# Kernel tuning notes

Hardware: AMD Instinct MI355X
Metric: run time of the kernel (lower is better)

## Reference

```python
import jax, jax.numpy as jnp
import numpy as np

N_NODES = 50000
N_EDGES = 400000
D_IN = 64
D_HID = 64
D_OUT = 64
NEG_SLOPE = 0.2   # GATConv LeakyReLU slope
BN_EPS = 1e-5


def _add_self_loops(row, col, N):
    loop = jnp.arange(N, dtype=row.dtype)
    return jnp.concatenate([row, loop]), jnp.concatenate([col, loop])


def _gcn_conv(x, row, col, N, W, b):
    # PyG GCNConv: add self loops, symmetric normalization, sum aggregate, bias
    r, c = _add_self_loops(row, col, N)
    deg = jax.ops.segment_sum(jnp.ones_like(r, dtype=x.dtype), c, num_segments=N)
    dis = jnp.where(deg > 0, deg ** -0.5, 0.0)
    norm = dis[r] * dis[c]                       # [E+N]
    h = x @ W                                    # [N, out]
    out = jax.ops.segment_sum(h[r] * norm[:, None], c, num_segments=N)
    return out + b


def _gat_conv(x, row, col, N, W, att_src, att_dst, b, concat):
    # PyG GATConv: per-edge attention with softmax over incoming edges
    H, C = att_src.shape
    r, c = _add_self_loops(row, col, N)
    h = (x @ W).reshape(N, H, C)
    a_src = jnp.einsum('nhc,hc->nh', h, att_src)
    a_dst = jnp.einsum('nhc,hc->nh', h, att_dst)
    e = jax.nn.leaky_relu(a_src[r] + a_dst[c], NEG_SLOPE)   # [E', H]
    m = jax.ops.segment_max(e, c, num_segments=N)           # stable softmax per target
    e = jnp.exp(e - m[c])
    denom = jax.ops.segment_sum(e, c, num_segments=N)
    alpha = e / denom[c]                                    # [E', H]
    out = jax.ops.segment_sum(h[r] * alpha[:, :, None], c, num_segments=N)  # [N,H,C]
    out = out.reshape(N, H * C) if concat else out.mean(axis=1)
    return out + b


def _sage_conv(x, row, col, N, Wl, bl, Wr):
    # PyG SAGEConv(aggr='mean', normalize=True): lin_l(mean_j x_j) + lin_r(x), then L2-normalize
    s = jax.ops.segment_sum(x[row], col, num_segments=N)
    cnt = jax.ops.segment_sum(jnp.ones_like(row, dtype=x.dtype), col, num_segments=N)
    mean = s / jnp.maximum(cnt, 1.0)[:, None]
    out = mean @ Wl + bl + x @ Wr
    n = jnp.linalg.norm(out, axis=-1, keepdims=True)
    return out / jnp.maximum(n, 1e-12)


def _forward(x, edge_index, gate_w1, gate_b1, gate_w2, gate_b2,
             gcn_w1, gcn_b1, bn_gamma, bn_beta, gcn_w2, gcn_b2,
             gat_w1, gat_att_src1, gat_att_dst1, gat_b1,
             gat_w2, gat_att_src2, gat_att_dst2, gat_b2,
             sage_wl1, sage_bl1, sage_wr1, sage_wl2, sage_bl2, sage_wr2):
    N = x.shape[0]
    row, col = edge_index[0], edge_index[1]
    # gate: mean node feature -> MLP -> softmax over 3 models
    g = jnp.mean(x, axis=0, keepdims=True)
    w = jax.nn.softmax(jax.nn.relu(g @ gate_w1 + gate_b1) @ gate_w2 + gate_b2, axis=-1)
    # GCN branch (eval: BatchNorm with running mean=0, var=1; dropout off)
    h = _gcn_conv(x, row, col, N, gcn_w1, gcn_b1)
    h = h * (bn_gamma / jnp.sqrt(1.0 + BN_EPS)) + bn_beta
    h = jax.nn.relu(h)
    out_gcn = _gcn_conv(h, row, col, N, gcn_w2, gcn_b2)
    # GAT branch: hidden layer 4 heads concat + ELU, output layer 1 head mean
    h = jax.nn.elu(_gat_conv(x, row, col, N, gat_w1, gat_att_src1, gat_att_dst1, gat_b1, True))
    out_gat = _gat_conv(h, row, col, N, gat_w2, gat_att_src2, gat_att_dst2, gat_b2, False)
    # SAGE branch
    h = jax.nn.relu(_sage_conv(x, row, col, N, sage_wl1, sage_bl1, sage_wr1))
    out_sage = _sage_conv(h, row, col, N, sage_wl2, sage_bl2, sage_wr2)
    return w[0, 0] * out_gcn + w[0, 1] * out_gat + w[0, 2] * out_sage


def setup_inputs() -> dict:
    key = jax.random.key(0)
    ks = jax.random.split(key, 16)
    def nrm(k, shape, scale=0.05):
        return jax.random.normal(k, shape, dtype=jnp.float32) * scale
    inp = {}
    inp['x'] = jax.random.normal(ks[0], (N_NODES, D_IN), dtype=jnp.float32)
    inp['edge_index'] = jax.random.randint(ks[1], (2, N_EDGES), 0, N_NODES, dtype=jnp.int32)
    inp['gate_w1'] = nrm(ks[2], (D_IN, 64)); inp['gate_b1'] = jnp.zeros((64,), jnp.float32)
    inp['gate_w2'] = nrm(ks[3], (64, 3));    inp['gate_b2'] = jnp.zeros((3,), jnp.float32)
    inp['gcn_w1'] = nrm(ks[4], (D_IN, D_HID)); inp['gcn_b1'] = jnp.zeros((D_HID,), jnp.float32)
    inp['bn_gamma'] = jnp.ones((D_HID,), jnp.float32); inp['bn_beta'] = jnp.zeros((D_HID,), jnp.float32)
    inp['gcn_w2'] = nrm(ks[5], (D_HID, D_OUT)); inp['gcn_b2'] = jnp.zeros((D_OUT,), jnp.float32)
    inp['gat_w1'] = nrm(ks[6], (D_IN, 4 * D_HID))
    inp['gat_att_src1'] = nrm(ks[7], (4, D_HID)); inp['gat_att_dst1'] = nrm(ks[8], (4, D_HID))
    inp['gat_b1'] = jnp.zeros((4 * D_HID,), jnp.float32)
    inp['gat_w2'] = nrm(ks[9], (4 * D_HID, D_OUT))
    inp['gat_att_src2'] = nrm(ks[10], (1, D_OUT)); inp['gat_att_dst2'] = nrm(ks[11], (1, D_OUT))
    inp['gat_b2'] = jnp.zeros((D_OUT,), jnp.float32)
    inp['sage_wl1'] = nrm(ks[12], (D_IN, D_HID)); inp['sage_bl1'] = jnp.zeros((D_HID,), jnp.float32)
    inp['sage_wr1'] = nrm(ks[13], (D_IN, D_HID))
    inp['sage_wl2'] = nrm(ks[14], (D_HID, D_OUT)); inp['sage_bl2'] = jnp.zeros((D_OUT,), jnp.float32)
    inp['sage_wr2'] = nrm(ks[15], (D_HID, D_OUT))
    return inp


def reference(x, edge_index, gate_w1, gate_b1, gate_w2, gate_b2,
              gcn_w1, gcn_b1, bn_gamma, bn_beta, gcn_w2, gcn_b2,
              gat_w1, gat_att_src1, gat_att_dst1, gat_b1,
              gat_w2, gat_att_src2, gat_att_dst2, gat_b2,
              sage_wl1, sage_bl1, sage_wr1, sage_wl2, sage_bl2, sage_wr2):
    return _forward(x, edge_index, gate_w1, gate_b1, gate_w2, gate_b2,
                    gcn_w1, gcn_b1, bn_gamma, bn_beta, gcn_w2, gcn_b2,
                    gat_w1, gat_att_src1, gat_att_dst1, gat_b1,
                    gat_w2, gat_att_src2, gat_att_dst2, gat_b2,
                    sage_wl1, sage_bl1, sage_wr1, sage_wl2, sage_bl2, sage_wr2)
```

## Files before the change

### kernel.cpp

```cpp
#include <hip/hip_runtime.h>
#include <hip/hip_bf16.h>
#include <math.h>

#define NN 50000
#define NE 400000

typedef __attribute__((ext_vector_type(8))) short bf16x8;
typedef __attribute__((ext_vector_type(4))) float f32x4;

__device__ __forceinline__ float lrelu(float v){ return v > 0.f ? v : 0.2f*v; }
__device__ __forceinline__ float elu1(float v){ return v > 0.f ? v : expm1f(v); }
__device__ __forceinline__ float bflo(unsigned int u){ return __uint_as_float(u << 16); }
__device__ __forceinline__ float bfhi(unsigned int u){ return __uint_as_float(u & 0xffff0000u); }
__device__ __forceinline__ unsigned short f2bf(float f){
  __hip_bfloat16 h = __float2bfloat16(f);
  return *(unsigned short*)&h;
}
__device__ __forceinline__ unsigned int pack2(float lo, float hi){
  return (unsigned int)f2bf(lo) | ((unsigned int)f2bf(hi) << 16);
}

__device__ __forceinline__ void stage_tab(unsigned short* Wt, const unsigned short* Wb, int tid){
  #pragma unroll
  for(int s = 0; s < 2; s++){
    int c = tid + s*256;
    int n = c >> 3, ko = (c & 7)*8;
    *(bf16x8*)&Wt[n*72 + ko] = *(const bf16x8*)&Wb[n*64 + ko];
  }
}

__global__ void k_count(const int* __restrict__ col, int* __restrict__ cnt, int E){
  int e = blockIdx.x*blockDim.x + threadIdx.x;
  if(e < E) atomicAdd(&cnt[col[e]], 1);
}

__global__ void k_alloc(const int* __restrict__ cnt, int* __restrict__ offs,
                        float* __restrict__ dis, float* __restrict__ invc,
                        int* __restrict__ total, int N){
  int i = blockIdx.x*blockDim.x + threadIdx.x;
  int lane = threadIdx.x & 63;
  int v = (i < N) ? cnt[i] : 0;
  int x = v;
  #pragma unroll
  for(int d = 1; d < 64; d <<= 1){ int t = __shfl_up(x, d, 64); if(lane >= d) x += t; }
  int base = 0;
  if(lane == 63 && x > 0) base = atomicAdd(total, x);
  base = __shfl(base, 63, 64);
  if(i < N){
    offs[i] = base + x - v;
    dis[i]  = 1.0f / sqrtf((float)(v + 1));
    invc[i] = 1.0f / fmaxf((float)v, 1.0f);
  }
}

__global__ void k_fill(const int* __restrict__ row, const int* __restrict__ col,
                       const int* __restrict__ offs, int* __restrict__ cursor,
                       int* __restrict__ csr, int E){
  int e = blockIdx.x*blockDim.x + threadIdx.x;
  if(e < E){
    int c = col[e];
    int pos = offs[c] + atomicAdd(&cursor[c], 1);
    csr[pos] = row[e];
  }
}

struct PKS { const float* src; unsigned short* dst; int kshift; int ldw; int col0; };
struct PKP { PKS s[11]; };

__global__ void k_packw(PKP p){
  PKS s = p.s[blockIdx.x];
  int K = 1 << s.kshift;
  int total = K << 6;
  for(int idx = threadIdx.x; idx < total; idx += 256){
    int n = idx >> s.kshift, k = idx & (K - 1);
    s.dst[idx] = f2bf(s.src[(size_t)k*s.ldw + s.col0 + n]);
  }
}

__global__ void k_castsum(const float* __restrict__ x, unsigned short* __restrict__ xb,
                          float* __restrict__ gsum, int N){
  __shared__ float part[4][64];
  int lane = threadIdx.x & 63, w = threadIdx.x >> 6;
  float s = 0.f;
  for(int r = blockIdx.x*4 + w; r < N; r += gridDim.x*4){
    float v = x[(size_t)r*64 + lane];
    xb[(size_t)r*64 + lane] = f2bf(v);
    s += v;
  }
  part[w][lane] = s;
  __syncthreads();
  if(w == 0) atomicAdd(&gsum[lane], part[0][lane]+part[1][lane]+part[2][lane]+part[3][lane]);
}

__global__ void k_gate(const float* __restrict__ gsum,
                       const float* __restrict__ w1, const float* __restrict__ b1,
                       const float* __restrict__ w2, const float* __restrict__ b2,
                       float* __restrict__ gatew){
  __shared__ float g[64]; __shared__ float hid[64]; __shared__ float lg[3];
  int t = threadIdx.x;
  g[t] = gsum[t] * (1.0f/(float)NN);
  __syncthreads();
  float acc = b1[t];
  for(int i = 0; i < 64; i++) acc += g[i]*w1[i*64 + t];
  hid[t] = fmaxf(acc, 0.f);
  __syncthreads();
  if(t < 3){
    float a = b2[t];
    for(int j = 0; j < 64; j++) a += hid[j]*w2[j*3 + t];
    lg[t] = a;
  }
  __syncthreads();
  if(t == 0){
    float m = fmaxf(lg[0], fmaxf(lg[1], lg[2]));
    float e0 = expf(lg[0]-m), e1 = expf(lg[1]-m), e2 = expf(lg[2]-m);
    float s = e0 + e1 + e2;
    gatew[0] = e0/s; gatew[1] = e1/s; gatew[2] = e2/s;
  }
}

__global__ void k_fold1(const float* __restrict__ w1, const float* __restrict__ as,
                        const float* __restrict__ ad, float* __restrict__ wsd){
  int t = threadIdx.x;
  int k = t & 63, h = t >> 6;
  float ssrc = 0.f, sdst = 0.f;
  for(int c = 0; c < 64; c++){
    float w = w1[k*256 + h*64 + c];
    ssrc += w * as[h*64 + c];
    sdst += w * ad[h*64 + c];
  }
  wsd[k*8 + h] = ssrc;
  wsd[k*8 + 4 + h] = sdst;
}

__global__ void k_attdotx(const unsigned short* __restrict__ xb, const float* __restrict__ wsd,
                          float* __restrict__ asrc, float* __restrict__ adst, int N){
  __shared__ float ws[64*8];
  int tid = threadIdx.x;
  ws[tid] = wsd[tid];
  ws[tid + 256] = wsd[tid + 256];
  __syncthreads();
  int node = blockIdx.x*16 + (tid >> 4);
  int l = tid & 15;
  if(node >= N) return;
  uint2 u = *(const uint2*)&xb[(size_t)node*64 + l*4];
  float v0 = bflo(u.x), v1 = bfhi(u.x), v2 = bflo(u.y), v3 = bfhi(u.y);
  float s[8];
  #pragma unroll
  for(int h = 0; h < 8; h++){
    s[h] = v0*ws[(l*4+0)*8+h] + v1*ws[(l*4+1)*8+h] + v2*ws[(l*4+2)*8+h] + v3*ws[(l*4+3)*8+h];
  }
  #pragma unroll
  for(int d = 8; d >= 1; d >>= 1){
    #pragma unroll
    for(int h = 0; h < 8; h++) s[h] += __shfl_xor(s[h], d, 16);
  }
  if(l == 0){
    float4 o1; o1.x = s[0]; o1.y = s[1]; o1.z = s[2]; o1.w = s[3];
    float4 o2; o2.x = s[4]; o2.y = s[5]; o2.z = s[6]; o2.w = s[7];
    *(float4*)&asrc[node*4] = o1;
    *(float4*)&adst[node*4] = o2;
  }
}

__global__ void k_edgew1(const float* __restrict__ asrc, const float* __restrict__ adst,
                         const int* __restrict__ offs, const int* __restrict__ cnt,
                         const int* __restrict__ csr,
                         float* __restrict__ wvE, float* __restrict__ rdenN,
                         float* __restrict__ wvS, int N){
  int node = blockIdx.x*4 + (threadIdx.x >> 6);
  int lane = threadIdx.x & 63;
  if(node >= N) return;
  float4 ad = *(const float4*)&adst[node*4];
  float a0 = 0.f, a1 = 0.f, a2 = 0.f, a3 = 0.f;
  int e0 = offs[node], e1 = e0 + cnt[node];
  for(int e = e0 + lane; e < e1; e += 64){
    int s = csr[e];
    float4 as = *(const float4*)&asrc[s*4];
    float4 w;
    w.x = expf(lrelu(as.x + ad.x));
    w.y = expf(lrelu(as.y + ad.y));
    w.z = expf(lrelu(as.z + ad.z));
    w.w = expf(lrelu(as.w + ad.w));
    a0 += w.x; a1 += w.y; a2 += w.z; a3 += w.w;
    *(float4*)&wvE[(size_t)e*4] = w;
  }
  #pragma unroll
  for(int d = 32; d >= 1; d >>= 1){
    a0 += __shfl_xor(a0, d, 64); a1 += __shfl_xor(a1, d, 64);
    a2 += __shfl_xor(a2, d, 64); a3 += __shfl_xor(a3, d, 64);
  }
  float4 asl = *(const float4*)&asrc[node*4];
  float4 ws;
  ws.x = expf(lrelu(asl.x + ad.x));
  ws.y = expf(lrelu(asl.y + ad.y));
  ws.z = expf(lrelu(asl.z + ad.z));
  ws.w = expf(lrelu(asl.w + ad.w));
  if(lane == 0){
    float4 rd;
    rd.x = 1.0f/(a0 + ws.x); rd.y = 1.0f/(a1 + ws.y);
    rd.z = 1.0f/(a2 + ws.z); rd.w = 1.0f/(a3 + ws.w);
    *(float4*)&rdenN[node*4] = rd;
    *(float4*)&wvS[node*4] = ws;
  }
}

__global__ void k_edgew2(const float* __restrict__ asrc, const float* __restrict__ adst,
                         const int* __restrict__ offs, const int* __restrict__ cnt,
                         const int* __restrict__ csr,
                         float* __restrict__ wvE, float* __restrict__ rdenN,
                         float* __restrict__ wvS, int N){
  int node = blockIdx.x*4 + (threadIdx.x >> 6);
  int lane = threadIdx.x & 63;
  if(node >= N) return;
  float ad = adst[node];
  float acc = 0.f;
  int e0 = offs[node], e1 = e0 + cnt[node];
  for(int e = e0 + lane; e < e1; e += 64){
    float w = expf(lrelu(asrc[csr[e]] + ad));
    acc += w;
    wvE[e] = w;
  }
  #pragma unroll
  for(int d = 32; d >= 1; d >>= 1) acc += __shfl_xor(acc, d, 64);
  float ws = expf(lrelu(asrc[node] + ad));
  if(lane == 0){
    rdenN[node] = 1.0f/(acc + ws);
    wvS[node] = ws;
  }
}

__global__ void k_aggx(const unsigned short* __restrict__ xb,
                       const float* __restrict__ wvE, const float* __restrict__ rden,
                       const float* __restrict__ wvS,
                       const float* __restrict__ dis, const float* __restrict__ invc,
                       const int* __restrict__ offs, const int* __restrict__ cnt,
                       const int* __restrict__ csr,
                       unsigned short* __restrict__ z, unsigned short* __restrict__ agcnx,
                       unsigned short* __restrict__ asagex, int N){
  int node = blockIdx.x*4 + (threadIdx.x >> 6);
  int lane = threadIdx.x & 63;
  if(node >= N) return;
  int half = lane >> 5, subl = lane & 31;
  float zg[4][2] = {{0,0},{0,0},{0,0},{0,0}};
  float gg[2] = {0,0}, ssv[2] = {0,0};
  int e0 = offs[node], e1 = e0 + cnt[node];
  #pragma unroll 2
  for(int e = e0 + half; e < e1; e += 2){
    int s = csr[e];
    float4 w4 = *(const float4*)&wvE[(size_t)e*4];
    float ds = dis[s];
    unsigned int u = *(const unsigned int*)&xb[(size_t)s*64 + subl*2];
    float xl = bflo(u), xh = bfhi(u);
    zg[0][0] = fmaf(w4.x, xl, zg[0][0]); zg[0][1] = fmaf(w4.x, xh, zg[0][1]);
    zg[1][0] = fmaf(w4.y, xl, zg[1][0]); zg[1][1] = fmaf(w4.y, xh, zg[1][1]);
    zg[2][0] = fmaf(w4.z, xl, zg[2][0]); zg[2][1] = fmaf(w4.z, xh, zg[2][1]);
    zg[3][0] = fmaf(w4.w, xl, zg[3][0]); zg[3][1] = fmaf(w4.w, xh, zg[3][1]);
    gg[0] = fmaf(ds, xl, gg[0]); gg[1] = fmaf(ds, xh, gg[1]);
    ssv[0] += xl; ssv[1] += xh;
  }
  #pragma unroll
  for(int h = 0; h < 4; h++){
    zg[h][0] += __shfl_xor(zg[h][0], 32, 64);
    zg[h][1] += __shfl_xor(zg[h][1], 32, 64);
  }
  gg[0] += __shfl_xor(gg[0], 32, 64); gg[1] += __shfl_xor(gg[1], 32, 64);
  ssv[0] += __shfl_xor(ssv[0], 32, 64); ssv[1] += __shfl_xor(ssv[1], 32, 64);
  if(half == 0){
    unsigned int un = *(const unsigned int*)&xb[(size_t)node*64 + subl*2];
    float xl = bflo(un), xh = bfhi(un);
    float4 ws4 = *(const float4*)&wvS[node*4];
    float4 rd4 = *(const float4*)&rden[node*4];
    unsigned int* zp = (unsigned int*)&z[(size_t)node*256 + subl*2];
    zp[0]   = pack2((zg[0][0] + ws4.x*xl)*rd4.x, (zg[0][1] + ws4.x*xh)*rd4.x);
    zp[32]  = pack2((zg[1][0] + ws4.y*xl)*rd4.y, (zg[1][1] + ws4.y*xh)*rd4.y);
    zp[64]  = pack2((zg[2][0] + ws4.z*xl)*rd4.z, (zg[2][1] + ws4.z*xh)*rd4.z);
    zp[96]  = pack2((zg[3][0] + ws4.w*xl)*rd4.w, (zg[3][1] + ws4.w*xh)*rd4.w);
    float dc = dis[node], ic = invc[node];
    *(unsigned int*)&agcnx[(size_t)node*64 + subl*2] =
        pack2(dc*fmaf(dc, xl, gg[0]), dc*fmaf(dc, xh, gg[1]));
    *(unsigned int*)&asagex[(size_t)node*64 + subl*2] = pack2(ssv[0]*ic, ssv[1]*ic);
  }
}

__global__ void k_aggf(const unsigned short* __restrict__ a1, const unsigned short* __restrict__ s1,
                       const unsigned short* __restrict__ h2,
                       const float* __restrict__ wvE, const float* __restrict__ rden,
                       const float* __restrict__ wvS,
                       const float* __restrict__ dis, const float* __restrict__ invc,
                       const int* __restrict__ offs, const int* __restrict__ cnt,
                       const int* __restrict__ csr,
                       unsigned short* __restrict__ A2agg, unsigned short* __restrict__ S2agg,
                       unsigned short* __restrict__ T2, int N){
  int node = blockIdx.x*4 + (threadIdx.x >> 6);
  int lane = threadIdx.x & 63;
  if(node >= N) return;
  int half = lane >> 5, subl = lane & 31;
  float aa[2] = {0,0}, ss[2] = {0,0}, tt[2] = {0,0};
  int e0 = offs[node], e1 = e0 + cnt[node];
  #pragma unroll 2
  for(int e = e0 + half; e < e1; e += 2){
    int s = csr[e];
    float ds = dis[s];
    float wv = wvE[e];
    unsigned int ua = *(const unsigned int*)&a1[(size_t)s*64 + subl*2];
    unsigned int us = *(const unsigned int*)&s1[(size_t)s*64 + subl*2];
    unsigned int uh = *(const unsigned int*)&h2[(size_t)s*64 + subl*2];
    aa[0] = fmaf(ds, bflo(ua), aa[0]); aa[1] = fmaf(ds, bfhi(ua), aa[1]);
    ss[0] += bflo(us); ss[1] += bfhi(us);
    tt[0] = fmaf(wv, bflo(uh), tt[0]); tt[1] = fmaf(wv, bfhi(uh), tt[1]);
  }
  aa[0] += __shfl_xor(aa[0], 32, 64); aa[1] += __shfl_xor(aa[1], 32, 64);
  ss[0] += __shfl_xor(ss[0], 32, 64); ss[1] += __shfl_xor(ss[1], 32, 64);
  tt[0] += __shfl_xor(tt[0], 32, 64); tt[1] += __shfl_xor(tt[1], 32, 64);
  if(half == 0){
    unsigned int uan = *(const unsigned int*)&a1[(size_t)node*64 + subl*2];
    unsigned int uhn = *(const unsigned int*)&h2[(size_t)node*64 + subl*2];
    float dc = dis[node], ic = invc[node];
    float rd = rden[node], wss = wvS[node];
    *(unsigned int*)&A2agg[(size_t)node*64 + subl*2] =
        pack2(dc*fmaf(dc, bflo(uan), aa[0]), dc*fmaf(dc, bfhi(uan), aa[1]));
    *(unsigned int*)&S2agg[(size_t)node*64 + subl*2] = pack2(ss[0]*ic, ss[1]*ic);
    *(unsigned int*)&T2[(size_t)node*64 + subl*2] =
        pack2(fmaf(wss, bflo(uhn), tt[0])*rd, fmaf(wss, bfhi(uhn), tt[1])*rd);
  }
}

struct MME {
  const unsigned short* A; const unsigned short* Wb;
  const unsigned short* A2; const unsigned short* Wb2;
  unsigned short* C;
  const float* b; const float* p1; const float* p2;
  int ep;
};
struct FSP {
  const unsigned short* z; const unsigned short* wb1; const float* b1;
  const unsigned short* wb2; const float* as2; const float* ad2;
  unsigned short* h2; float* asrc2; float* adst2;
  MME mm[2];
  int N;
};

__global__ __launch_bounds__(256, 4) void k_fused1(FSP p){
  __shared__ unsigned short smem[16896];
  const int N = p.N;
  int tid = threadIdx.x;
  int w = tid >> 6, lane = tid & 63, quad = lane >> 4, m16 = lane & 15;
  int rowa = blockIdx.x*64 + w*16 + m16;
  int rowc = rowa < N ? rowa : N - 1;
  int robase = blockIdx.x*64 + w*16 + quad*4;

  if(blockIdx.y == 0){
    unsigned short* GH = smem;
    int lr = w*16;
    #pragma unroll
    for(int h = 0; h < 4; h++){
      bf16x8 a0 = *(const bf16x8*)&p.z[(size_t)rowc*256 + h*64 + quad*8];
      bf16x8 a1 = *(const bf16x8*)&p.z[(size_t)rowc*256 + h*64 + 32 + quad*8];
      f32x4 acc[4];
      #pragma unroll
      for(int t = 0; t < 4; t++){ acc[t][0]=0.f; acc[t][1]=0.f; acc[t][2]=0.f; acc[t][3]=0.f; }
      #pragma unroll
      for(int t = 0; t < 4; t++){
        const unsigned short* wb = p.wb1 + (size_t)h*4096 + (t*16 + m16)*64;
        bf16x8 b0 = *(const bf16x8*)&wb[quad*8];
        bf16x8 b1v = *(const bf16x8*)&wb[32 + quad*8];
        acc[t] = __builtin_amdgcn_mfma_f32_16x16x32_bf16(a0, b0, acc[t], 0, 0, 0);
        acc[t] = __builtin_amdgcn_mfma_f32_16x16x32_bf16(a1, b1v, acc[t], 0, 0, 0);
      }
      #pragma unroll
      for(int t = 0; t < 4; t++){
        float bv = p.b1[h*64 + t*16 + m16];
        #pragma unroll
        for(int r = 0; r < 4; r++){
          GH[(lr + quad*4 + r)*264 + h*64 + t*16 + m16] = f2bf(elu1(acc[t][r] + bv));
        }
      }
    }
    __syncthreads();
    f32x4 acc2[4];
    #pragma unroll
    for(int t = 0; t < 4; t++){ acc2[t][0]=0.f; acc2[t][1]=0.f; acc2[t][2]=0.f; acc2[t][3]=0.f; }
    #pragma unroll
    for(int kc = 0; kc < 256; kc += 64){
      bf16x8 a0 = *(const bf16x8*)&GH[(lr + m16)*264 + kc + quad*8];
      bf16x8 a1 = *(const bf16x8*)&GH[(lr + m16)*264 + kc + 32 + quad*8];
      #pragma unroll
      for(int t = 0; t < 4; t++){
        const unsigned short* wb = p.wb2 + (size_t)(t*16 + m16)*256 + kc;
        bf16x8 b0 = *(const bf16x8*)&wb[quad*8];
        bf16x8 b1v = *(const bf16x8*)&wb[32 + quad*8];
        acc2[t] = __builtin_amdgcn_mfma_f32_16x16x32_bf16(a0, b0, acc2[t], 0, 0, 0);
        acc2[t] = __builtin_amdgcn_mfma_f32_16x16x32_bf16(a1, b1v, acc2[t], 0, 0, 0);
      }
    }
    #pragma unroll
    for(int t = 0; t < 4; t++){
      int col = t*16 + m16;
      #pragma unroll
      for(int r = 0; r < 4; r++){
        int ro = robase + r;
        if(ro < N) p.h2[(size_t)ro*64 + col] = f2bf(acc2[t][r]);
      }
    }
    float ps[4] = {0,0,0,0}, pd[4] = {0,0,0,0};
    #pragma unroll
    for(int t = 0; t < 4; t++){
      int col = t*16 + m16;
      float a_ = p.as2[col], d_ = p.ad2[col];
      #pragma unroll
      for(int r = 0; r < 4; r++){ ps[r] = fmaf(acc2[t][r], a_, ps[r]); pd[r] = fmaf(acc2[t][r], d_, pd[r]); }
    }
    #pragma unroll
    for(int d = 8; d >= 1; d >>= 1){
      #pragma unroll
      for(int r = 0; r < 4; r++){ ps[r] += __shfl_xor(ps[r], d, 64); pd[r] += __shfl_xor(pd[r], d, 64); }
    }
    if(m16 == 0){
      #pragma unroll
      for(int r = 0; r < 4; r++){
        int ro = robase + r;
        if(ro < N){ p.asrc2[ro] = ps[r]; p.adst2[ro] = pd[r]; }
      }
    }
    return;
  }

  MME m = p.mm[blockIdx.y - 1];
  unsigned short* Wt  = smem;
  unsigned short* Wt2 = smem + 4608;
  stage_tab(Wt, m.Wb, tid);
  if(m.Wb2) stage_tab(Wt2, m.Wb2, tid);
  __syncthreads();
  f32x4 acc[4];
  #pragma unroll
  for(int t = 0; t < 4; t++){ acc[t][0]=0.f; acc[t][1]=0.f; acc[t][2]=0.f; acc[t][3]=0.f; }
  {
    bf16x8 a0 = *(const bf16x8*)&m.A[(size_t)rowc*64 + quad*8];
    bf16x8 a1 = *(const bf16x8*)&m.A[(size_t)rowc*64 + 32 + quad*8];
    #pragma unroll
    for(int t = 0; t < 4; t++){
      bf16x8 b0 = *(const bf16x8*)&Wt[(t*16 + m16)*72 + quad*8];
      bf16x8 b1 = *(const bf16x8*)&Wt[(t*16 + m16)*72 + 32 + quad*8];
      acc[t] = __builtin_amdgcn_mfma_f32_16x16x32_bf16(a0, b0, acc[t], 0, 0, 0);
      acc[t] = __builtin_amdgcn_mfma_f32_16x16x32_bf16(a1, b1, acc[t], 0, 0, 0);
    }
  }
  if(m.A2){
    bf16x8 a0 = *(const bf16x8*)&m.A2[(size_t)rowc*64 + quad*8];
    bf16x8 a1 = *(const bf16x8*)&m.A2[(size_t)rowc*64 + 32 + quad*8];
    #pragma unroll
    for(int t = 0; t < 4; t++){
      bf16x8 b0 = *(const bf16x8*)&Wt2[(t*16 + m16)*72 + quad*8];
      bf16x8 b1 = *(const bf16x8*)&Wt2[(t*16 + m16)*72 + 32 + quad*8];
      acc[t] = __builtin_amdgcn_mfma_f32_16x16x32_bf16(a0, b0, acc[t], 0, 0, 0);
      acc[t] = __builtin_amdgcn_mfma_f32_16x16x32_bf16(a1, b1, acc[t], 0, 0, 0);
    }
  }
  if(m.ep == 3){
    float v[4][4], n2[4] = {0,0,0,0};
    #pragma unroll
    for(int t = 0; t < 4; t++){
      float bv = m.b[t*16 + m16];
      #pragma unroll
      for(int r = 0; r < 4; r++){ v[t][r] = acc[t][r] + bv; n2[r] = fmaf(v[t][r], v[t][r], n2[r]); }
    }
    #pragma unroll
    for(int d = 8; d >= 1; d >>= 1){
      #pragma unroll
      for(int r = 0; r < 4; r++) n2[r] += __shfl_xor(n2[r], d, 64);
    }
    float inv[4];
    #pragma unroll
    for(int r = 0; r < 4; r++) inv[r] = 1.0f / fmaxf(sqrtf(n2[r]), 1e-12f);
    #pragma unroll
    for(int t = 0; t < 4; t++){
      #pragma unroll
      for(int r = 0; r < 4; r++){
        int ro = robase + r;
        if(ro < N) m.C[(size_t)ro*64 + t*16 + m16] = f2bf(fmaxf(v[t][r]*inv[r], 0.f));
      }
    }
    return;
  }
  #pragma unroll
  for(int t = 0; t < 4; t++){
    int col = t*16 + m16;
    float bv = m.b[col];
    float gm = m.p1[col]*rsqrtf(1.0f + 1e-5f);
    float be = m.p2[col];
    #pragma unroll
    for(int r = 0; r < 4; r++){
      int ro = robase + r;
      if(ro < N){
        m.C[(size_t)ro*64 + col] = f2bf(fmaxf((acc[t][r] + bv)*gm + be, 0.f));
      }
    }
  }
}

__global__ __launch_bounds__(256) void k_mm_final(
    const unsigned short* __restrict__ A2agg, const unsigned short* __restrict__ wb_gcn2,
    const float* __restrict__ gcn_b2,
    const unsigned short* __restrict__ S2agg, const unsigned short* __restrict__ wb_wl2,
    const float* __restrict__ bl2,
    const unsigned short* __restrict__ s1, const unsigned short* __restrict__ wb_wr2,
    const unsigned short* __restrict__ T2, const float* __restrict__ gat_b2,
    const float* __restrict__ gatew, float* __restrict__ out, int N){
  __shared__ unsigned short W1s[64*72];
  __shared__ unsigned short W2s[64*72];
  __shared__ unsigned short W3s[64*72];
  int tid = threadIdx.x;
  stage_tab(W1s, wb_gcn2, tid);
  stage_tab(W2s, wb_wl2, tid);
  stage_tab(W3s, wb_wr2, tid);
  __syncthreads();
  int w = tid >> 6, lane = tid & 63, quad = lane >> 4, m16 = lane & 15;
  int rowa = blockIdx.x*64 + w*16 + m16;
  int rowc = rowa < N ? rowa : N - 1;
  f32x4 accg[4], accs[4];
  #pragma unroll
  for(int t = 0; t < 4; t++){
    accg[t][0]=0.f; accg[t][1]=0.f; accg[t][2]=0.f; accg[t][3]=0.f;
    accs[t][0]=0.f; accs[t][1]=0.f; accs[t][2]=0.f; accs[t][3]=0.f;
  }
  {
    bf16x8 a0 = *(const bf16x8*)&A2agg[(size_t)rowc*64 + quad*8];
    bf16x8 a1 = *(const bf16x8*)&A2agg[(size_t)rowc*64 + 32 + quad*8];
    #pragma unroll
    for(int t = 0; t < 4; t++){
      bf16x8 b0 = *(const bf16x8*)&W1s[(t*16 + m16)*72 + quad*8];
      bf16x8 b1 = *(const bf16x8*)&W1s[(t*16 + m16)*72 + 32 + quad*8];
      accg[t] = __builtin_amdgcn_mfma_f32_16x16x32_bf16(a0, b0, accg[t], 0, 0, 0);
      accg[t] = __builtin_amdgcn_mfma_f32_16x16x32_bf16(a1, b1, accg[t], 0, 0, 0);
    }
  }
  {
    bf16x8 a0 = *(const bf16x8*)&S2agg[(size_t)rowc*64 + quad*8];
    bf16x8 a1 = *(const bf16x8*)&S2agg[(size_t)rowc*64 + 32 + quad*8];
    #pragma unroll
    for(int t = 0; t < 4; t++){
      bf16x8 b0 = *(const bf16x8*)&W2s[(t*16 + m16)*72 + quad*8];
      bf16x8 b1 = *(const bf16x8*)&W2s[(t*16 + m16)*72 + 32 + quad*8];
      accs[t] = __builtin_amdgcn_mfma_f32_16x16x32_bf16(a0, b0, accs[t], 0, 0, 0);
      accs[t] = __builtin_amdgcn_mfma_f32_16x16x32_bf16(a1, b1, accs[t], 0, 0, 0);
    }
  }
  {
    bf16x8 a0 = *(const bf16x8*)&s1[(size_t)rowc*64 + quad*8];
    bf16x8 a1 = *(const bf16x8*)&s1[(size_t)rowc*64 + 32 + quad*8];
    #pragma unroll
    for(int t = 0; t < 4; t++){
      bf16x8 b0 = *(const bf16x8*)&W3s[(t*16 + m16)*72 + quad*8];
      bf16x8 b1 = *(const bf16x8*)&W3s[(t*16 + m16)*72 + 32 + quad*8];
      accs[t] = __builtin_amdgcn_mfma_f32_16x16x32_bf16(a0, b0, accs[t], 0, 0, 0);
      accs[t] = __builtin_amdgcn_mfma_f32_16x16x32_bf16(a1, b1, accs[t], 0, 0, 0);
    }
  }
  float w0 = gatew[0], w1 = gatew[1], w2 = gatew[2];
  int robase = blockIdx.x*64 + w*16 + quad*4;
  float vs[4][4], n2[4] = {0,0,0,0};
  #pragma unroll
  for(int t = 0; t < 4; t++){
    float bsv = bl2[t*16 + m16];
    #pragma unroll
    for(int r = 0; r < 4; r++){ vs[t][r] = accs[t][r] + bsv; n2[r] = fmaf(vs[t][r], vs[t][r], n2[r]); }
  }
  #pragma unroll
  for(int d = 8; d >= 1; d >>= 1){
    #pragma unroll
    for(int r = 0; r < 4; r++) n2[r] += __shfl_xor(n2[r], d, 64);
  }
  float inv[4];
  #pragma unroll
  for(int r = 0; r < 4; r++) inv[r] = 1.0f / fmaxf(sqrtf(n2[r]), 1e-12f);
  #pragma unroll
  for(int t = 0; t < 4; t++){
    int col = t*16 + m16;
    float bg = gcn_b2[col], bt = gat_b2[col];
    #pragma unroll
    for(int r = 0; r < 4; r++){
      int ro = robase + r;
      if(ro < N){
        float t2 = bflo((unsigned int)T2[(size_t)ro*64 + col]);
        out[(size_t)ro*64 + col] = w0*(accg[t][r] + bg) + w1*(t2 + bt) + w2*vs[t][r]*inv[r];
      }
    }
  }
}

extern "C" void kernel_launch(void* const* d_in, const int* in_sizes, int n_in,
                              void* d_out, int out_size, void* d_ws, size_t ws_size,
                              hipStream_t stream){
  const float* x        = (const float*)d_in[0];
  const int*   ei       = (const int*)d_in[1];
  const int*   row      = ei;
  const int*   col      = ei + NE;
  const float* gate_w1  = (const float*)d_in[2];
  const float* gate_b1  = (const float*)d_in[3];
  const float* gate_w2  = (const float*)d_in[4];
  const float* gate_b2  = (const float*)d_in[5];
  const float* gcn_w1   = (const float*)d_in[6];
  const float* gcn_b1   = (const float*)d_in[7];
  const float* bn_gamma = (const float*)d_in[8];
  const float* bn_beta  = (const float*)d_in[9];
  const float* gcn_w2   = (const float*)d_in[10];
  const float* gcn_b2   = (const float*)d_in[11];
  const float* gat_w1   = (const float*)d_in[12];
  const float* gat_as1  = (const float*)d_in[13];
  const float* gat_ad1  = (const float*)d_in[14];
  const float* gat_b1   = (const float*)d_in[15];
  const float* gat_w2   = (const float*)d_in[16];
  const float* gat_as2  = (const float*)d_in[17];
  const float* gat_ad2  = (const float*)d_in[18];
  const float* gat_b2   = (const float*)d_in[19];
  const float* sage_wl1 = (const float*)d_in[20];
  const float* sage_bl1 = (const float*)d_in[21];
  const float* sage_wr1 = (const float*)d_in[22];
  const float* sage_wl2 = (const float*)d_in[23];
  const float* sage_bl2 = (const float*)d_in[24];
  const float* sage_wr2 = (const float*)d_in[25];
  float* out = (float*)d_out;

  char* wp = (char*)d_ws;
  auto alloc = [&](size_t bytes)->char*{ char* p = wp; wp += (bytes + 255) & ~(size_t)255; return p; };
  int*   cnt    = (int*)  alloc((size_t)NN*4);
  int*   cursor = (int*)  alloc((size_t)NN*4);
  float* gsum   = (float*)alloc(64*4);
  int*   total  = (int*)  alloc(256);
  size_t zbytes = (size_t)(wp - (char*)cnt);
  int*   offs   = (int*)  alloc((size_t)NN*4);
  int*   csr    = (int*)  alloc((size_t)NE*4);
  float* dis    = (float*)alloc((size_t)NN*4);
  float* invc   = (float*)alloc((size_t)NN*4);
  float* gatew  = (float*)alloc(16);
  float* wsd    = (float*)alloc(64*8*4);
  float* asrc1  = (float*)alloc((size_t)NN*4*4);
  float* adst1  = (float*)alloc((size_t)NN*4*4);
  float* asrc2  = (float*)alloc((size_t)NN*4);
  float* adst2  = (float*)alloc((size_t)NN*4);
  float* wvE1   = (float*)alloc((size_t)NE*4*4);
  float* rden1  = (float*)alloc((size_t)NN*4*4);
  float* wvS1   = (float*)alloc((size_t)NN*4*4);
  float* wvE2   = (float*)alloc((size_t)NE*4);
  float* rden2  = (float*)alloc((size_t)NN*4);
  float* wvS2   = (float*)alloc((size_t)NN*4);
  unsigned short* xb     = (unsigned short*)alloc((size_t)NN*64*2);
  unsigned short* z      = (unsigned short*)alloc((size_t)NN*256*2);
  unsigned short* agcnx  = (unsigned short*)alloc((size_t)NN*64*2);
  unsigned short* asagex = (unsigned short*)alloc((size_t)NN*64*2);
  unsigned short* a1     = (unsigned short*)alloc((size_t)NN*64*2);
  unsigned short* s1     = (unsigned short*)alloc((size_t)NN*64*2);
  unsigned short* h2     = (unsigned short*)alloc((size_t)NN*64*2);
  unsigned short* A2agg  = (unsigned short*)alloc((size_t)NN*64*2);
  unsigned short* S2agg  = (unsigned short*)alloc((size_t)NN*64*2);
  unsigned short* T2     = (unsigned short*)alloc((size_t)NN*64*2);
  unsigned short* wb_gcn1 = (unsigned short*)alloc((size_t)64*64*2);
  unsigned short* wb_wl1  = (unsigned short*)alloc((size_t)64*64*2);
  unsigned short* wb_wr1  = (unsigned short*)alloc((size_t)64*64*2);
  unsigned short* wb_gat1 = (unsigned short*)alloc((size_t)256*64*2);
  unsigned short* wb_gat2 = (unsigned short*)alloc((size_t)64*256*2);
  unsigned short* wb_gcn2 = (unsigned short*)alloc((size_t)64*64*2);
  unsigned short* wb_wl2  = (unsigned short*)alloc((size_t)64*64*2);
  unsigned short* wb_wr2  = (unsigned short*)alloc((size_t)64*64*2);

  hipMemsetAsync(cnt, 0, zbytes, stream);

  const int gN  = (NN + 63) / 64;
  const int g4  = NN / 4;
  const int g16 = NN / 16;
  const int gA  = (NN + 255) / 256;

  {
    PKP pk = {};
    pk.s[0]  = {gcn_w1,   wb_gcn1,            6, 64,  0};
    pk.s[1]  = {sage_wl1, wb_wl1,             6, 64,  0};
    pk.s[2]  = {sage_wr1, wb_wr1,             6, 64,  0};
    pk.s[3]  = {gat_w1,   wb_gat1 + 0*64*64,  6, 256, 0};
    pk.s[4]  = {gat_w1,   wb_gat1 + 1*64*64,  6, 256, 64};
    pk.s[5]  = {gat_w1,   wb_gat1 + 2*64*64,  6, 256, 128};
    pk.s[6]  = {gat_w1,   wb_gat1 + 3*64*64,  6, 256, 192};
    pk.s[7]  = {gat_w2,   wb_gat2,            8, 64,  0};
    pk.s[8]  = {gcn_w2,   wb_gcn2,            6, 64,  0};
    pk.s[9]  = {sage_wl2, wb_wl2,             6, 64,  0};
    pk.s[10] = {sage_wr2, wb_wr2,             6, 64,  0};
    k_packw<<<11, 256, 0, stream>>>(pk);
  }

  k_count<<<(NE+255)/256, 256, 0, stream>>>(col, cnt, NE);
  k_alloc<<<gA, 256, 0, stream>>>(cnt, offs, dis, invc, total, NN);
  k_fill <<<(NE+255)/256, 256, 0, stream>>>(row, col, offs, cursor, csr, NE);
  k_castsum<<<256, 256, 0, stream>>>(x, xb, gsum, NN);
  k_gate  <<<1, 64, 0, stream>>>(gsum, gate_w1, gate_b1, gate_w2, gate_b2, gatew);
  k_fold1 <<<1, 256, 0, stream>>>(gat_w1, gat_as1, gat_ad1, wsd);
  k_attdotx<<<g16, 256, 0, stream>>>(xb, wsd, asrc1, adst1, NN);
  k_edgew1<<<g4, 256, 0, stream>>>(asrc1, adst1, offs, cnt, csr, wvE1, rden1, wvS1, NN);

  k_aggx<<<g4, 256, 0, stream>>>(xb, wvE1, rden1, wvS1, dis, invc, offs, cnt, csr,
                                 z, agcnx, asagex, NN);

  {
    FSP p = {};
    p.N = NN;
    p.z = z; p.wb1 = wb_gat1; p.b1 = gat_b1;
    p.wb2 = wb_gat2; p.as2 = gat_as2; p.ad2 = gat_ad2;
    p.h2 = h2; p.asrc2 = asrc2; p.adst2 = adst2;
    p.mm[0] = {agcnx, wb_gcn1, nullptr, nullptr, a1, gcn_b1, bn_gamma, bn_beta, 1};
    p.mm[1] = {asagex, wb_wl1, xb, wb_wr1, s1, sage_bl1, nullptr, nullptr, 3};
    k_fused1<<<dim3(gN,3), 256, 0, stream>>>(p);
  }

  k_edgew2<<<g4, 256, 0, stream>>>(asrc2, adst2, offs, cnt, csr, wvE2, rden2, wvS2, NN);

  k_aggf<<<g4, 256, 0, stream>>>(a1, s1, h2, wvE2, rden2, wvS2, dis, invc,
                                 offs, cnt, csr, A2agg, S2agg, T2, NN);

  k_mm_final<<<gN, 256, 0, stream>>>(A2agg, wb_gcn2, gcn_b2, S2agg, wb_wl2, sage_bl2,
                                     s1, wb_wr2, T2, gat_b2, gatew, out, NN);
}
```

Measured before the change: 361.9 us.

## Fuse edge-weight, aggregation and matmul stages into two mega kernels

Merges the GAT edge-weight computation, neighbor aggregation and the dense layer matmuls for each layer into one kernel per layer. Softmax weights are recomputed inline during aggregation, and intermediate aggregates are kept in shared memory instead of going through global buffers. This removes several launches and the global round-trips of per-edge weights and aggregated features. In exchange, each wave processes 16 nodes serially and the launch-bounds occupancy drops, which may reduce parallelism in the memory-bound gather phase.

```diff
diff --git a/kernel.cpp b/kernel.cpp
--- a/kernel.cpp
+++ b/kernel.cpp
@@ -18,15 +18,6 @@
 }
 __device__ __forceinline__ unsigned int pack2(float lo, float hi){
   return (unsigned int)f2bf(lo) | ((unsigned int)f2bf(hi) << 16);
-}
-
-__device__ __forceinline__ void stage_tab(unsigned short* Wt, const unsigned short* Wb, int tid){
-  #pragma unroll
-  for(int s = 0; s < 2; s++){
-    int c = tid + s*256;
-    int n = c >> 3, ko = (c & 7)*8;
-    *(bf16x8*)&Wt[n*72 + ko] = *(const bf16x8*)&Wb[n*64 + ko];
-  }
 }
 
 __global__ void k_count(const int* __restrict__ col, int* __restrict__ cnt, int E){
@@ -162,427 +153,375 @@
   }
 }
 
-__global__ void k_edgew1(const float* __restrict__ asrc, const float* __restrict__ adst,
-                         const int* __restrict__ offs, const int* __restrict__ cnt,
-                         const int* __restrict__ csr,
-                         float* __restrict__ wvE, float* __restrict__ rdenN,
-                         float* __restrict__ wvS, int N){
-  int node = blockIdx.x*4 + (threadIdx.x >> 6);
-  int lane = threadIdx.x & 63;
-  if(node >= N) return;
-  float4 ad = *(const float4*)&adst[node*4];
-  float a0 = 0.f, a1 = 0.f, a2 = 0.f, a3 = 0.f;
-  int e0 = offs[node], e1 = e0 + cnt[node];
-  for(int e = e0 + lane; e < e1; e += 64){
-    int s = csr[e];
-    float4 as = *(const float4*)&asrc[s*4];
-    float4 w;
-    w.x = expf(lrelu(as.x + ad.x));
-    w.y = expf(lrelu(as.y + ad.y));
-    w.z = expf(lrelu(as.z + ad.z));
-    w.w = expf(lrelu(as.w + ad.w));
-    a0 += w.x; a1 += w.y; a2 += w.z; a3 += w.w;
-    *(float4*)&wvE[(size_t)e*4] = w;
-  }
-  #pragma unroll
-  for(int d = 32; d >= 1; d >>= 1){
-    a0 += __shfl_xor(a0, d, 64); a1 += __shfl_xor(a1, d, 64);
-    a2 += __shfl_xor(a2, d, 64); a3 += __shfl_xor(a3, d, 64);
-  }
-  float4 asl = *(const float4*)&asrc[node*4];
-  float4 ws;
-  ws.x = expf(lrelu(asl.x + ad.x));
-  ws.y = expf(lrelu(asl.y + ad.y));
-  ws.z = expf(lrelu(asl.z + ad.z));
-  ws.w = expf(lrelu(asl.w + ad.w));
-  if(lane == 0){
-    float4 rd;
-    rd.x = 1.0f/(a0 + ws.x); rd.y = 1.0f/(a1 + ws.y);
-    rd.z = 1.0f/(a2 + ws.z); rd.w = 1.0f/(a3 + ws.w);
-    *(float4*)&rdenN[node*4] = rd;
-    *(float4*)&wvS[node*4] = ws;
-  }
-}
-
-__global__ void k_edgew2(const float* __restrict__ asrc, const float* __restrict__ adst,
-                         const int* __restrict__ offs, const int* __restrict__ cnt,
-                         const int* __restrict__ csr,
-                         float* __restrict__ wvE, float* __restrict__ rdenN,
-                         float* __restrict__ wvS, int N){
-  int node = blockIdx.x*4 + (threadIdx.x >> 6);
-  int lane = threadIdx.x & 63;
-  if(node >= N) return;
-  float ad = adst[node];
-  float acc = 0.f;
-  int e0 = offs[node], e1 = e0 + cnt[node];
-  for(int e = e0 + lane; e < e1; e += 64){
-    float w = expf(lrelu(asrc[csr[e]] + ad));
-    acc += w;
-    wvE[e] = w;
-  }
-  #pragma unroll
-  for(int d = 32; d >= 1; d >>= 1) acc += __shfl_xor(acc, d, 64);
-  float ws = expf(lrelu(asrc[node] + ad));
-  if(lane == 0){
-    rdenN[node] = 1.0f/(acc + ws);
-    wvS[node] = ws;
-  }
-}
-
-__global__ void k_aggx(const unsigned short* __restrict__ xb,
-                       const float* __restrict__ wvE, const float* __restrict__ rden,
-                       const float* __restrict__ wvS,
-                       const float* __restrict__ dis, const float* __restrict__ invc,
-                       const int* __restrict__ offs, const int* __restrict__ cnt,
-                       const int* __restrict__ csr,
-                       unsigned short* __restrict__ z, unsigned short* __restrict__ agcnx,
-                       unsigned short* __restrict__ asagex, int N){
-  int node = blockIdx.x*4 + (threadIdx.x >> 6);
-  int lane = threadIdx.x & 63;
-  if(node >= N) return;
-  int half = lane >> 5, subl = lane & 31;
-  float zg[4][2] = {{0,0},{0,0},{0,0},{0,0}};
-  float gg[2] = {0,0}, ssv[2] = {0,0};
-  int e0 = offs[node], e1 = e0 + cnt[node];
-  #pragma unroll 2
-  for(int e = e0 + half; e < e1; e += 2){
-    int s = csr[e];
-    float4 w4 = *(const float4*)&wvE[(size_t)e*4];
-    float ds = dis[s];
-    unsigned int u = *(const unsigned int*)&xb[(size_t)s*64 + subl*2];
-    float xl = bflo(u), xh = bfhi(u);
-    zg[0][0] = fmaf(w4.x, xl, zg[0][0]); zg[0][1] = fmaf(w4.x, xh, zg[0][1]);
-    zg[1][0] = fmaf(w4.y, xl, zg[1][0]); zg[1][1] = fmaf(w4.y, xh, zg[1][1]);
-    zg[2][0] = fmaf(w4.z, xl, zg[2][0]); zg[2][1] = fmaf(w4.z, xh, zg[2][1]);
-    zg[3][0] = fmaf(w4.w, xl, zg[3][0]); zg[3][1] = fmaf(w4.w, xh, zg[3][1]);
-    gg[0] = fmaf(ds, xl, gg[0]); gg[1] = fmaf(ds, xh, gg[1]);
-    ssv[0] += xl; ssv[1] += xh;
-  }
-  #pragma unroll
-  for(int h = 0; h < 4; h++){
-    zg[h][0] += __shfl_xor(zg[h][0], 32, 64);
-    zg[h][1] += __shfl_xor(zg[h][1], 32, 64);
-  }
-  gg[0] += __shfl_xor(gg[0], 32, 64); gg[1] += __shfl_xor(gg[1], 32, 64);
-  ssv[0] += __shfl_xor(ssv[0], 32, 64); ssv[1] += __shfl_xor(ssv[1], 32, 64);
-  if(half == 0){
-    unsigned int un = *(const unsigned int*)&xb[(size_t)node*64 + subl*2];
-    float xl = bflo(un), xh = bfhi(un);
-    float4 ws4 = *(const float4*)&wvS[node*4];
-    float4 rd4 = *(const float4*)&rden[node*4];
-    unsigned int* zp = (unsigned int*)&z[(size_t)node*256 + subl*2];
-    zp[0]   = pack2((zg[0][0] + ws4.x*xl)*rd4.x, (zg[0][1] + ws4.x*xh)*rd4.x);
-    zp[32]  = pack2((zg[1][0] + ws4.y*xl)*rd4.y, (zg[1][1] + ws4.y*xh)*rd4.y);
-    zp[64]  = pack2((zg[2][0] + ws4.z*xl)*rd4.z, (zg[2][1] + ws4.z*xh)*rd4.z);
-    zp[96]  = pack2((zg[3][0] + ws4.w*xl)*rd4.w, (zg[3][1] + ws4.w*xh)*rd4.w);
-    float dc = dis[node], ic = invc[node];
-    *(unsigned int*)&agcnx[(size_t)node*64 + subl*2] =
-        pack2(dc*fmaf(dc, xl, gg[0]), dc*fmaf(dc, xh, gg[1]));
-    *(unsigned int*)&asagex[(size_t)node*64 + subl*2] = pack2(ssv[0]*ic, ssv[1]*ic);
-  }
-}
-
-__global__ void k_aggf(const unsigned short* __restrict__ a1, const unsigned short* __restrict__ s1,
-                       const unsigned short* __restrict__ h2,
-                       const float* __restrict__ wvE, const float* __restrict__ rden,
-                       const float* __restrict__ wvS,
-                       const float* __restrict__ dis, const float* __restrict__ invc,
-                       const int* __restrict__ offs, const int* __restrict__ cnt,
-                       const int* __restrict__ csr,
-                       unsigned short* __restrict__ A2agg, unsigned short* __restrict__ S2agg,
-                       unsigned short* __restrict__ T2, int N){
-  int node = blockIdx.x*4 + (threadIdx.x >> 6);
-  int lane = threadIdx.x & 63;
-  if(node >= N) return;
-  int half = lane >> 5, subl = lane & 31;
-  float aa[2] = {0,0}, ss[2] = {0,0}, tt[2] = {0,0};
-  int e0 = offs[node], e1 = e0 + cnt[node];
-  #pragma unroll 2
-  for(int e = e0 + half; e < e1; e += 2){
-    int s = csr[e];
-    float ds = dis[s];
-    float wv = wvE[e];
-    unsigned int ua = *(const unsigned int*)&a1[(size_t)s*64 + subl*2];
-    unsigned int us = *(const unsigned int*)&s1[(size_t)s*64 + subl*2];
-    unsigned int uh = *(const unsigned int*)&h2[(size_t)s*64 + subl*2];
-    aa[0] = fmaf(ds, bflo(ua), aa[0]); aa[1] = fmaf(ds, bfhi(ua), aa[1]);
-    ss[0] += bflo(us); ss[1] += bfhi(us);
-    tt[0] = fmaf(wv, bflo(uh), tt[0]); tt[1] = fmaf(wv, bfhi(uh), tt[1]);
-  }
-  aa[0] += __shfl_xor(aa[0], 32, 64); aa[1] += __shfl_xor(aa[1], 32, 64);
-  ss[0] += __shfl_xor(ss[0], 32, 64); ss[1] += __shfl_xor(ss[1], 32, 64);
-  tt[0] += __shfl_xor(tt[0], 32, 64); tt[1] += __shfl_xor(tt[1], 32, 64);
-  if(half == 0){
-    unsigned int uan = *(const unsigned int*)&a1[(size_t)node*64 + subl*2];
-    unsigned int uhn = *(const unsigned int*)&h2[(size_t)node*64 + subl*2];
-    float dc = dis[node], ic = invc[node];
-    float rd = rden[node], wss = wvS[node];
-    *(unsigned int*)&A2agg[(size_t)node*64 + subl*2] =
-        pack2(dc*fmaf(dc, bflo(uan), aa[0]), dc*fmaf(dc, bfhi(uan), aa[1]));
-    *(unsigned int*)&S2agg[(size_t)node*64 + subl*2] = pack2(ss[0]*ic, ss[1]*ic);
-    *(unsigned int*)&T2[(size_t)node*64 + subl*2] =
-        pack2(fmaf(wss, bflo(uhn), tt[0])*rd, fmaf(wss, bfhi(uhn), tt[1])*rd);
-  }
-}
-
-struct MME {
-  const unsigned short* A; const unsigned short* Wb;
-  const unsigned short* A2; const unsigned short* Wb2;
-  unsigned short* C;
-  const float* b; const float* p1; const float* p2;
-  int ep;
-};
-struct FSP {
-  const unsigned short* z; const unsigned short* wb1; const float* b1;
-  const unsigned short* wb2; const float* as2; const float* ad2;
-  unsigned short* h2; float* asrc2; float* adst2;
-  MME mm[2];
+struct M1P {
+  const unsigned short* xb;
+  const float* asrc1; const float* adst1;
+  const int* offs; const int* cnt; const int* csr;
+  const float* dis; const float* invc;
+  const unsigned short* wb_gcn1; const float* gcn_b1; const float* bn_gamma; const float* bn_beta;
+  const unsigned short* wb_wl1; const float* sage_bl1; const unsigned short* wb_wr1;
+  const unsigned short* wb_gat1; const float* gat_b1;
+  const unsigned short* wb_gat2; const float* gat_as2; const float* gat_ad2;
+  unsigned short* a1; unsigned short* s1; unsigned short* h2;
+  float* asrc2; float* adst2;
   int N;
 };
 
-__global__ __launch_bounds__(256, 4) void k_fused1(FSP p){
-  __shared__ unsigned short smem[16896];
+__global__ __launch_bounds__(256, 3) void k_mega1(M1P p){
+  __shared__ unsigned short Z[64*264];
+  __shared__ unsigned short AG[64*72];
+  __shared__ unsigned short AS[64*72];
   const int N = p.N;
   int tid = threadIdx.x;
   int w = tid >> 6, lane = tid & 63, quad = lane >> 4, m16 = lane & 15;
-  int rowa = blockIdx.x*64 + w*16 + m16;
+  int half = lane >> 5, subl = lane & 31;
+
+  for(int i = 0; i < 16; i++){
+    int node = blockIdx.x*64 + (w<<4) + i;
+    if(node >= N) break;
+    int lw = (w<<4) + i;
+    float4 ad4 = *(const float4*)&p.adst1[node*4];
+    float zg[4][2] = {{0,0},{0,0},{0,0},{0,0}};
+    float gg[2] = {0,0}, ssv[2] = {0,0}, wsum[4] = {0,0,0,0};
+    int e0 = p.offs[node], e1 = e0 + p.cnt[node];
+    #pragma unroll 2
+    for(int e = e0 + half; e < e1; e += 2){
+      int s = p.csr[e];
+      float4 as4 = *(const float4*)&p.asrc1[s*4];
+      float ds = p.dis[s];
+      unsigned int u = *(const unsigned int*)&p.xb[(size_t)s*64 + subl*2];
+      float w0 = expf(lrelu(as4.x + ad4.x));
+      float w1 = expf(lrelu(as4.y + ad4.y));
+      float w2 = expf(lrelu(as4.z + ad4.z));
+      float w3 = expf(lrelu(as4.w + ad4.w));
+      float xl = bflo(u), xh = bfhi(u);
+      zg[0][0] = fmaf(w0, xl, zg[0][0]); zg[0][1] = fmaf(w0, xh, zg[0][1]);
+      zg[1][0] = fmaf(w1, xl, zg[1][0]); zg[1][1] = fmaf(w1, xh, zg[1][1]);
+      zg[2][0] = fmaf(w2, xl, zg[2][0]); zg[2][1] = fmaf(w2, xh, zg[2][1]);
+      zg[3][0] = fmaf(w3, xl, zg[3][0]); zg[3][1] = fmaf(w3, xh, zg[3][1]);
+      gg[0] = fmaf(ds, xl, gg[0]); gg[1] = fmaf(ds, xh, gg[1]);
+      ssv[0] += xl; ssv[1] += xh;
+      wsum[0] += w0; wsum[1] += w1; wsum[2] += w2; wsum[3] += w3;
+    }
+    #pragma unroll
+    for(int h = 0; h < 4; h++){
+      zg[h][0] += __shfl_xor(zg[h][0], 32, 64);
+      zg[h][1] += __shfl_xor(zg[h][1], 32, 64);
+      wsum[h]  += __shfl_xor(wsum[h], 32, 64);
+    }
+    gg[0] += __shfl_xor(gg[0], 32, 64); gg[1] += __shfl_xor(gg[1], 32, 64);
+    ssv[0] += __shfl_xor(ssv[0], 32, 64); ssv[1] += __shfl_xor(ssv[1], 32, 64);
+    if(half == 0){
+      unsigned int un = *(const unsigned int*)&p.xb[(size_t)node*64 + subl*2];
+      float xl = bflo(un), xh = bfhi(un);
+      float4 asn = *(const float4*)&p.asrc1[node*4];
+      float s0 = expf(lrelu(asn.x + ad4.x));
+      float s1v = expf(lrelu(asn.y + ad4.y));
+      float s2 = expf(lrelu(asn.z + ad4.z));
+      float s3 = expf(lrelu(asn.w + ad4.w));
+      float rd0 = 1.0f/(wsum[0] + s0), rd1 = 1.0f/(wsum[1] + s1v);
+      float rd2 = 1.0f/(wsum[2] + s2), rd3 = 1.0f/(wsum[3] + s3);
+      unsigned int* zp = (unsigned int*)&Z[lw*264 + subl*2];
+      zp[0]  = pack2((zg[0][0] + s0*xl)*rd0,  (zg[0][1] + s0*xh)*rd0);
+      zp[32] = pack2((zg[1][0] + s1v*xl)*rd1, (zg[1][1] + s1v*xh)*rd1);
+      zp[64] = pack2((zg[2][0] + s2*xl)*rd2,  (zg[2][1] + s2*xh)*rd2);
+      zp[96] = pack2((zg[3][0] + s3*xl)*rd3,  (zg[3][1] + s3*xh)*rd3);
+      float dc = p.dis[node], ic = p.invc[node];
+      *(unsigned int*)&AG[lw*72 + subl*2] =
+          pack2(dc*fmaf(dc, xl, gg[0]), dc*fmaf(dc, xh, gg[1]));
+      *(unsigned int*)&AS[lw*72 + subl*2] = pack2(ssv[0]*ic, ssv[1]*ic);
+    }
+  }
+
+  int rowa = blockIdx.x*64 + (w<<4) + m16;
   int rowc = rowa < N ? rowa : N - 1;
-  int robase = blockIdx.x*64 + w*16 + quad*4;
-
-  if(blockIdx.y == 0){
-    unsigned short* GH = smem;
-    int lr = w*16;
-    #pragma unroll
-    for(int h = 0; h < 4; h++){
-      bf16x8 a0 = *(const bf16x8*)&p.z[(size_t)rowc*256 + h*64 + quad*8];
-      bf16x8 a1 = *(const bf16x8*)&p.z[(size_t)rowc*256 + h*64 + 32 + quad*8];
-      f32x4 acc[4];
-      #pragma unroll
-      for(int t = 0; t < 4; t++){ acc[t][0]=0.f; acc[t][1]=0.f; acc[t][2]=0.f; acc[t][3]=0.f; }
-      #pragma unroll
-      for(int t = 0; t < 4; t++){
-        const unsigned short* wb = p.wb1 + (size_t)h*4096 + (t*16 + m16)*64;
-        bf16x8 b0 = *(const bf16x8*)&wb[quad*8];
-        bf16x8 b1v = *(const bf16x8*)&wb[32 + quad*8];
-        acc[t] = __builtin_amdgcn_mfma_f32_16x16x32_bf16(a0, b0, acc[t], 0, 0, 0);
-        acc[t] = __builtin_amdgcn_mfma_f32_16x16x32_bf16(a1, b1v, acc[t], 0, 0, 0);
-      }
-      #pragma unroll
-      for(int t = 0; t < 4; t++){
-        float bv = p.b1[h*64 + t*16 + m16];
-        #pragma unroll
-        for(int r = 0; r < 4; r++){
-          GH[(lr + quad*4 + r)*264 + h*64 + t*16 + m16] = f2bf(elu1(acc[t][r] + bv));
-        }
-      }
-    }
-    __syncthreads();
-    f32x4 acc2[4];
-    #pragma unroll
-    for(int t = 0; t < 4; t++){ acc2[t][0]=0.f; acc2[t][1]=0.f; acc2[t][2]=0.f; acc2[t][3]=0.f; }
-    #pragma unroll
-    for(int kc = 0; kc < 256; kc += 64){
-      bf16x8 a0 = *(const bf16x8*)&GH[(lr + m16)*264 + kc + quad*8];
-      bf16x8 a1 = *(const bf16x8*)&GH[(lr + m16)*264 + kc + 32 + quad*8];
-      #pragma unroll
-      for(int t = 0; t < 4; t++){
-        const unsigned short* wb = p.wb2 + (size_t)(t*16 + m16)*256 + kc;
-        bf16x8 b0 = *(const bf16x8*)&wb[quad*8];
-        bf16x8 b1v = *(const bf16x8*)&wb[32 + quad*8];
-        acc2[t] = __builtin_amdgcn_mfma_f32_16x16x32_bf16(a0, b0, acc2[t], 0, 0, 0);
-        acc2[t] = __builtin_amdgcn_mfma_f32_16x16x32_bf16(a1, b1v, acc2[t], 0, 0, 0);
-      }
+  int lrow = (w<<4) + m16;
+  int robase = blockIdx.x*64 + (w<<4) + quad*4;
+
+  {
+    bf16x8 a0 = *(const bf16x8*)&AG[lrow*72 + quad*8];
+    bf16x8 a1v = *(const bf16x8*)&AG[lrow*72 + 32 + quad*8];
+    f32x4 acc[4];
+    #pragma unroll
+    for(int t = 0; t < 4; t++){ acc[t][0]=0.f; acc[t][1]=0.f; acc[t][2]=0.f; acc[t][3]=0.f; }
+    #pragma unroll
+    for(int t = 0; t < 4; t++){
+      const unsigned short* wb = p.wb_gcn1 + (size_t)(t*16 + m16)*64;
+      bf16x8 b0 = *(const bf16x8*)&wb[quad*8];
+      bf16x8 b1 = *(const bf16x8*)&wb[32 + quad*8];
+      acc[t] = __builtin_amdgcn_mfma_f32_16x16x32_bf16(a0, b0, acc[t], 0, 0, 0);
+      acc[t] = __builtin_amdgcn_mfma_f32_16x16x32_bf16(a1v, b1, acc[t], 0, 0, 0);
     }
     #pragma unroll
     for(int t = 0; t < 4; t++){
       int col = t*16 + m16;
+      float bv = p.gcn_b1[col];
+      float gm = p.bn_gamma[col]*rsqrtf(1.0f + 1e-5f);
+      float be = p.bn_beta[col];
       #pragma unroll
       for(int r = 0; r < 4; r++){
         int ro = robase + r;
-        if(ro < N) p.h2[(size_t)ro*64 + col] = f2bf(acc2[t][r]);
+        if(ro < N) p.a1[(size_t)ro*64 + col] = f2bf(fmaxf((acc[t][r] + bv)*gm + be, 0.f));
       }
     }
-    float ps[4] = {0,0,0,0}, pd[4] = {0,0,0,0};
-    #pragma unroll
-    for(int t = 0; t < 4; t++){
-      int col = t*16 + m16;
-      float a_ = p.as2[col], d_ = p.ad2[col];
+  }
+
+  {
+    f32x4 acc[4];
+    #pragma unroll
+    for(int t = 0; t < 4; t++){ acc[t][0]=0.f; acc[t][1]=0.f; acc[t][2]=0.f; acc[t][3]=0.f; }
+    {
+      bf16x8 a0 = *(const bf16x8*)&AS[lrow*72 + quad*8];
+      bf16x8 a1v = *(const bf16x8*)&AS[lrow*72 + 32 + quad*8];
       #pragma unroll
-      for(int r = 0; r < 4; r++){ ps[r] = fmaf(acc2[t][r], a_, ps[r]); pd[r] = fmaf(acc2[t][r], d_, pd[r]); }
+      for(int t = 0; t < 4; t++){
+        const unsigned short* wb = p.wb_wl1 + (size_t)(t*16 + m16)*64;
+        bf16x8 b0 = *(const bf16x8*)&wb[quad*8];
+        bf16x8 b1 = *(const bf16x8*)&wb[32 + quad*8];
+        acc[t] = __builtin_amdgcn_mfma_f32_16x16x32_bf16(a0, b0, acc[t], 0, 0, 0);
+        acc[t] = __builtin_amdgcn_mfma_f32_16x16x32_bf16(a1v, b1, acc[t], 0, 0, 0);
+      }
+    }
+    {
+      bf16x8 a0 = *(const bf16x8*)&p.xb[(size_t)rowc*64 + quad*8];
+      bf16x8 a1v = *(const bf16x8*)&p.xb[(size_t)rowc*64 + 32 + quad*8];
+      #pragma unroll
+      for(int t = 0; t < 4; t++){
+        const unsigned short* wb = p.wb_wr1 + (size_t)(t*16 + m16)*64;
+        bf16x8 b0 = *(const bf16x8*)&wb[quad*8];
+        bf16x8 b1 = *(const bf16x8*)&wb[32 + quad*8];
+        acc[t] = __builtin_amdgcn_mfma_f32_16x16x32_bf16(a0, b0, acc[t], 0, 0, 0);
+        acc[t] = __builtin_amdgcn_mfma_f32_16x16x32_bf16(a1v, b1, acc[t], 0, 0, 0);
+      }
+    }
+    float v[4][4], n2[4] = {0,0,0,0};
+    #pragma unroll
+    for(int t = 0; t < 4; t++){
+      float bv = p.sage_bl1[t*16 + m16];
+      #pragma unroll
+      for(int r = 0; r < 4; r++){ v[t][r] = acc[t][r] + bv; n2[r] = fmaf(v[t][r], v[t][r], n2[r]); }
     }
     #pragma unroll
     for(int d = 8; d >= 1; d >>= 1){
       #pragma unroll
-      for(int r = 0; r < 4; r++){ ps[r] += __shfl_xor(ps[r], d, 64); pd[r] += __shfl_xor(pd[r], d, 64); }
-    }
-    if(m16 == 0){
+      for(int r = 0; r < 4; r++) n2[r] += __shfl_xor(n2[r], d, 64);
+    }
+    float inv[4];
+    #pragma unroll
+    for(int r = 0; r < 4; r++) inv[r] = 1.0f / fmaxf(sqrtf(n2[r]), 1e-12f);
+    #pragma unroll
+    for(int t = 0; t < 4; t++){
       #pragma unroll
       for(int r = 0; r < 4; r++){
         int ro = robase + r;
-        if(ro < N){ p.asrc2[ro] = ps[r]; p.adst2[ro] = pd[r]; }
+        if(ro < N) p.s1[(size_t)ro*64 + t*16 + m16] = f2bf(fmaxf(v[t][r]*inv[r], 0.f));
       }
     }
-    return;
-  }
-
-  MME m = p.mm[blockIdx.y - 1];
-  unsigned short* Wt  = smem;
-  unsigned short* Wt2 = smem + 4608;
-  stage_tab(Wt, m.Wb, tid);
-  if(m.Wb2) stage_tab(Wt2, m.Wb2, tid);
-  __syncthreads();
-  f32x4 acc[4];
-  #pragma unroll
-  for(int t = 0; t < 4; t++){ acc[t][0]=0.f; acc[t][1]=0.f; acc[t][2]=0.f; acc[t][3]=0.f; }
-  {
-    bf16x8 a0 = *(const bf16x8*)&m.A[(size_t)rowc*64 + quad*8];
-    bf16x8 a1 = *(const bf16x8*)&m.A[(size_t)rowc*64 + 32 + quad*8];
-    #pragma unroll
-    for(int t = 0; t < 4; t++){
-      bf16x8 b0 = *(const bf16x8*)&Wt[(t*16 + m16)*72 + quad*8];
-      bf16x8 b1 = *(const bf16x8*)&Wt[(t*16 + m16)*72 + 32 + quad*8];
+  }
+
+  int lr = w << 4;
+  #pragma unroll
+  for(int h = 0; h < 4; h++){
+    bf16x8 a0 = *(const bf16x8*)&Z[lrow*264 + h*64 + quad*8];
+    bf16x8 a1v = *(const bf16x8*)&Z[lrow*264 + h*64 + 32 + quad*8];
+    f32x4 acc[4];
+    #pragma unroll
+    for(int t = 0; t < 4; t++){ acc[t][0]=0.f; acc[t][1]=0.f; acc[t][2]=0.f; acc[t][3]=0.f; }
+    #pragma unroll
+    for(int t = 0; t < 4; t++){
+      const unsigned short* wb = p.wb_gat1 + (size_t)h*4096 + (size_t)(t*16 + m16)*64;
+      bf16x8 b0 = *(const bf16x8*)&wb[quad*8];
+      bf16x8 b1 = *(const bf16x8*)&wb[32 + quad*8];
       acc[t] = __builtin_amdgcn_mfma_f32_16x16x32_bf16(a0, b0, acc[t], 0, 0, 0);
-      acc[t] = __builtin_amdgcn_mfma_f32_16x16x32_bf16(a1, b1, acc[t], 0, 0, 0);
-    }
-  }
-  if(m.A2){
-    bf16x8 a0 = *(const bf16x8*)&m.A2[(size_t)rowc*64 + quad*8];
-    bf16x8 a1 = *(const bf16x8*)&m.A2[(size_t)rowc*64 + 32 + quad*8];
-    #pragma unroll
-    for(int t = 0; t < 4; t++){
-      bf16x8 b0 = *(const bf16x8*)&Wt2[(t*16 + m16)*72 + quad*8];
-      bf16x8 b1 = *(const bf16x8*)&Wt2[(t*16 + m16)*72 + 32 + quad*8];
-      acc[t] = __builtin_amdgcn_mfma_f32_16x16x32_bf16(a0, b0, acc[t], 0, 0, 0);
-      acc[t] = __builtin_amdgcn_mfma_f32_16x16x32_bf16(a1, b1, acc[t], 0, 0, 0);
-    }
-  }
-  if(m.ep == 3){
-    float v[4][4], n2[4] = {0,0,0,0};
-    #pragma unroll
-    for(int t = 0; t < 4; t++){
-      float bv = m.b[t*16 + m16];
-      #pragma unroll
-      for(int r = 0; r < 4; r++){ v[t][r] = acc[t][r] + bv; n2[r] = fmaf(v[t][r], v[t][r], n2[r]); }
-    }
-    #pragma unroll
-    for(int d = 8; d >= 1; d >>= 1){
-      #pragma unroll
-      for(int r = 0; r < 4; r++) n2[r] += __shfl_xor(n2[r], d, 64);
-    }
-    float inv[4];
-    #pragma unroll
-    for(int r = 0; r < 4; r++) inv[r] = 1.0f / fmaxf(sqrtf(n2[r]), 1e-12f);
-    #pragma unroll
-    for(int t = 0; t < 4; t++){
+      acc[t] = __builtin_amdgcn_mfma_f32_16x16x32_bf16(a1v, b1, acc[t], 0, 0, 0);
+    }
+    #pragma unroll
+    for(int t = 0; t < 4; t++){
+      float bv = p.gat_b1[h*64 + t*16 + m16];
       #pragma unroll
       for(int r = 0; r < 4; r++){
-        int ro = robase + r;
-        if(ro < N) m.C[(size_t)ro*64 + t*16 + m16] = f2bf(fmaxf(v[t][r]*inv[r], 0.f));
+        Z[(lr + quad*4 + r)*264 + h*64 + t*16 + m16] = f2bf(elu1(acc[t][r] + bv));
       }
     }
-    return;
+  }
+
+  f32x4 acc2[4];
+  #pragma unroll
+  for(int t = 0; t < 4; t++){ acc2[t][0]=0.f; acc2[t][1]=0.f; acc2[t][2]=0.f; acc2[t][3]=0.f; }
+  #pragma unroll
+  for(int kc = 0; kc < 256; kc += 64){
+    bf16x8 a0 = *(const bf16x8*)&Z[lrow*264 + kc + quad*8];
+    bf16x8 a1v = *(const bf16x8*)&Z[lrow*264 + kc + 32 + quad*8];
+    #pragma unroll
+    for(int t = 0; t < 4; t++){
+      const unsigned short* wb = p.wb_gat2 + (size_t)(t*16 + m16)*256 + kc;
+      bf16x8 b0 = *(const bf16x8*)&wb[quad*8];
+      bf16x8 b1 = *(const bf16x8*)&wb[32 + quad*8];
+      acc2[t] = __builtin_amdgcn_mfma_f32_16x16x32_bf16(a0, b0, acc2[t], 0, 0, 0);
+      acc2[t] = __builtin_amdgcn_mfma_f32_16x16x32_bf16(a1v, b1, acc2[t], 0, 0, 0);
+    }
   }
   #pragma unroll
   for(int t = 0; t < 4; t++){
     int col = t*16 + m16;
-    float bv = m.b[col];
-    float gm = m.p1[col]*rsqrtf(1.0f + 1e-5f);
-    float be = m.p2[col];
+    #pragma unroll
+    for(int r = 0; r < 4; r++){
+      int ro = robase + r;
+      if(ro < N) p.h2[(size_t)ro*64 + col] = f2bf(acc2[t][r]);
+    }
+  }
+  float ps[4] = {0,0,0,0}, pd[4] = {0,0,0,0};
+  #pragma unroll
+  for(int t = 0; t < 4; t++){
+    int col = t*16 + m16;
+    float a_ = p.gat_as2[col], d_ = p.gat_ad2[col];
+    #pragma unroll
+    for(int r = 0; r < 4; r++){ ps[r] = fmaf(acc2[t][r], a_, ps[r]); pd[r] = fmaf(acc2[t][r], d_, pd[r]); }
+  }
+  #pragma unroll
+  for(int d = 8; d >= 1; d >>= 1){
+    #pragma unroll
+    for(int r = 0; r < 4; r++){ ps[r] += __shfl_xor(ps[r], d, 64); pd[r] += __shfl_xor(pd[r], d, 64); }
+  }
+  if(m16 == 0){
+    #pragma unroll
+    for(int r = 0; r < 4; r++){
+      int ro = robase + r;
+      if(ro < N){ p.asrc2[ro] = ps[r]; p.adst2[ro] = pd[r]; }
+    }
+  }
+}
+
+struct M2P {
+  const unsigned short* a1; const unsigned short* s1; const unsigned short* h2;
+  const float* asrc2; const float* adst2;
+  const int* offs; const int* cnt; const int* csr;
+  const float* dis; const float* invc;
+  const unsigned short* wb_gcn2; const float* gcn_b2;
+  const unsigned short* wb_wl2; const float* bl2; const unsigned short* wb_wr2;
+  const float* gat_b2; const float* gatew;
+  float* out; int N;
+};
+
+__global__ __launch_bounds__(256, 4) void k_mega2(M2P p){
+  __shared__ unsigned short A2[64*72];
+  __shared__ unsigned short S2[64*72];
+  __shared__ unsigned short T2[64*72];
+  const int N = p.N;
+  int tid = threadIdx.x;
+  int w = tid >> 6, lane = tid & 63, quad = lane >> 4, m16 = lane & 15;
+  int half = lane >> 5, subl = lane & 31;
+
+  for(int i = 0; i < 16; i++){
+    int node = blockIdx.x*64 + (w<<4) + i;
+    if(node >= N) break;
+    int lw = (w<<4) + i;
+    float ad = p.adst2[node];
+    float aa[2] = {0,0}, ss[2] = {0,0}, tt[2] = {0,0}, wsum = 0.f;
+    int e0 = p.offs[node], e1 = e0 + p.cnt[node];
+    #pragma unroll 2
+    for(int e = e0 + half; e < e1; e += 2){
+      int s = p.csr[e];
+      float wv = expf(lrelu(p.asrc2[s] + ad));
+      float ds = p.dis[s];
+      unsigned int ua = *(const unsigned int*)&p.a1[(size_t)s*64 + subl*2];
+      unsigned int us = *(const unsigned int*)&p.s1[(size_t)s*64 + subl*2];
+      unsigned int uh = *(const unsigned int*)&p.h2[(size_t)s*64 + subl*2];
+      aa[0] = fmaf(ds, bflo(ua), aa[0]); aa[1] = fmaf(ds, bfhi(ua), aa[1]);
+      ss[0] += bflo(us); ss[1] += bfhi(us);
+      tt[0] = fmaf(wv, bflo(uh), tt[0]); tt[1] = fmaf(wv, bfhi(uh), tt[1]);
+      wsum += wv;
+    }
+    aa[0] += __shfl_xor(aa[0], 32, 64); aa[1] += __shfl_xor(aa[1], 32, 64);
+    ss[0] += __shfl_xor(ss[0], 32, 64); ss[1] += __shfl_xor(ss[1], 32, 64);
+    tt[0] += __shfl_xor(tt[0], 32, 64); tt[1] += __shfl_xor(tt[1], 32, 64);
+    wsum  += __shfl_xor(wsum, 32, 64);
+    if(half == 0){
+      float wss = expf(lrelu(p.asrc2[node] + ad));
+      float rd = 1.0f/(wsum + wss);
+      unsigned int uan = *(const unsigned int*)&p.a1[(size_t)node*64 + subl*2];
+      unsigned int uhn = *(const unsigned int*)&p.h2[(size_t)node*64 + subl*2];
+      float dc = p.dis[node], ic = p.invc[node];
+      *(unsigned int*)&A2[lw*72 + subl*2] =
+          pack2(dc*fmaf(dc, bflo(uan), aa[0]), dc*fmaf(dc, bfhi(uan), aa[1]));
+      *(unsigned int*)&S2[lw*72 + subl*2] = pack2(ss[0]*ic, ss[1]*ic);
+      *(unsigned int*)&T2[lw*72 + subl*2] =
+          pack2(fmaf(wss, bflo(uhn), tt[0])*rd, fmaf(wss, bfhi(uhn), tt[1])*rd);
+    }
+  }
+
+  int rowa = blockIdx.x*64 + (w<<4) + m16;
+  int rowc = rowa < N ? rowa : N - 1;
+  int lrow = (w<<4) + m16;
+  int robase = blockIdx.x*64 + (w<<4) + quad*4;
+  f32x4 accg[4], accs[4];
+  #pragma unroll
+  for(int t = 0; t < 4; t++){
+    accg[t][0]=0.f; accg[t][1]=0.f; accg[t][2]=0.f; accg[t][3]=0.f;
+    accs[t][0]=0.f; accs[t][1]=0.f; accs[t][2]=0.f; accs[t][3]=0.f;
+  }
+  {
+    bf16x8 a0 = *(const bf16x8*)&A2[lrow*72 + quad*8];
+    bf16x8 a1v = *(const bf16x8*)&A2[lrow*72 + 32 + quad*8];
+    #pragma unroll
+    for(int t = 0; t < 4; t++){
+      const unsigned short* wb = p.wb_gcn2 + (size_t)(t*16 + m16)*64;
+      bf16x8 b0 = *(const bf16x8*)&wb[quad*8];
+      bf16x8 b1 = *(const bf16x8*)&wb[32 + quad*8];
+      accg[t] = __builtin_amdgcn_mfma_f32_16x16x32_bf16(a0, b0, accg[t], 0, 0, 0);
+      accg[t] = __builtin_amdgcn_mfma_f32_16x16x32_bf16(a1v, b1, accg[t], 0, 0, 0);
+    }
+  }
+  {
+    bf16x8 a0 = *(const bf16x8*)&S2[lrow*72 + quad*8];
+    bf16x8 a1v = *(const bf16x8*)&S2[lrow*72 + 32 + quad*8];
+    #pragma unroll
+    for(int t = 0; t < 4; t++){
+      const unsigned short* wb = p.wb_wl2 + (size_t)(t*16 + m16)*64;
+      bf16x8 b0 = *(const bf16x8*)&wb[quad*8];
+      bf16x8 b1 = *(const bf16x8*)&wb[32 + quad*8];
+      accs[t] = __builtin_amdgcn_mfma_f32_16x16x32_bf16(a0, b0, accs[t], 0, 0, 0);
+      accs[t] = __builtin_amdgcn_mfma_f32_16x16x32_bf16(a1v, b1, accs[t], 0, 0, 0);
+    }
+  }
+  {
+    bf16x8 a0 = *(const bf16x8*)&p.s1[(size_t)rowc*64 + quad*8];
+    bf16x8 a1v = *(const bf16x8*)&p.s1[(size_t)rowc*64 + 32 + quad*8];
+    #pragma unroll
+    for(int t = 0; t < 4; t++){
+      const unsigned short* wb = p.wb_wr2 + (size_t)(t*16 + m16)*64;
+      bf16x8 b0 = *(const bf16x8*)&wb[quad*8];
+      bf16x8 b1 = *(const bf16x8*)&wb[32 + quad*8];
+      accs[t] = __builtin_amdgcn_mfma_f32_16x16x32_bf16(a0, b0, accs[t], 0, 0, 0);
+      accs[t] = __builtin_amdgcn_mfma_f32_16x16x32_bf16(a1v, b1, accs[t], 0, 0, 0);
+    }
+  }
+  float w0 = p.gatew[0], w1 = p.gatew[1], w2 = p.gatew[2];
+  float vs[4][4], n2[4] = {0,0,0,0};
+  #pragma unroll
+  for(int t = 0; t < 4; t++){
+    float bsv = p.bl2[t*16 + m16];
+    #pragma unroll
+    for(int r = 0; r < 4; r++){ vs[t][r] = accs[t][r] + bsv; n2[r] = fmaf(vs[t][r], vs[t][r], n2[r]); }
+  }
+  #pragma unroll
+  for(int d = 8; d >= 1; d >>= 1){
+    #pragma unroll
+    for(int r = 0; r < 4; r++) n2[r] += __shfl_xor(n2[r], d, 64);
+  }
+  float inv[4];
+  #pragma unroll
+  for(int r = 0; r < 4; r++) inv[r] = 1.0f / fmaxf(sqrtf(n2[r]), 1e-12f);
+  #pragma unroll
+  for(int t = 0; t < 4; t++){
+    int col = t*16 + m16;
+    float bg = p.gcn_b2[col], bt = p.gat_b2[col];
     #pragma unroll
     for(int r = 0; r < 4; r++){
       int ro = robase + r;
       if(ro < N){
-        m.C[(size_t)ro*64 + col] = f2bf(fmaxf((acc[t][r] + bv)*gm + be, 0.f));
-      }
-    }
-  }
-}
-
-__global__ __launch_bounds__(256) void k_mm_final(
-    const unsigned short* __restrict__ A2agg, const unsigned short* __restrict__ wb_gcn2,
-    const float* __restrict__ gcn_b2,
-    const unsigned short* __restrict__ S2agg, const unsigned short* __restrict__ wb_wl2,
-    const float* __restrict__ bl2,
-    const unsigned short* __restrict__ s1, const unsigned short* __restrict__ wb_wr2,
-    const unsigned short* __restrict__ T2, const float* __restrict__ gat_b2,
-    const float* __restrict__ gatew, float* __restrict__ out, int N){
-  __shared__ unsigned short W1s[64*72];
-  __shared__ unsigned short W2s[64*72];
-  __shared__ unsigned short W3s[64*72];
-  int tid = threadIdx.x;
-  stage_tab(W1s, wb_gcn2, tid);
-  stage_tab(W2s, wb_wl2, tid);
-  stage_tab(W3s, wb_wr2, tid);
-  __syncthreads();
-  int w = tid >> 6, lane = tid & 63, quad = lane >> 4, m16 = lane & 15;
-  int rowa = blockIdx.x*64 + w*16 + m16;
-  int rowc = rowa < N ? rowa : N - 1;
-  f32x4 accg[4], accs[4];
-  #pragma unroll
-  for(int t = 0; t < 4; t++){
-    accg[t][0]=0.f; accg[t][1]=0.f; accg[t][2]=0.f; accg[t][3]=0.f;
-    accs[t][0]=0.f; accs[t][1]=0.f; accs[t][2]=0.f; accs[t][3]=0.f;
-  }
-  {
-    bf16x8 a0 = *(const bf16x8*)&A2agg[(size_t)rowc*64 + quad*8];
-    bf16x8 a1 = *(const bf16x8*)&A2agg[(size_t)rowc*64 + 32 + quad*8];
-    #pragma unroll
-    for(int t = 0; t < 4; t++){
-      bf16x8 b0 = *(const bf16x8*)&W1s[(t*16 + m16)*72 + quad*8];
-      bf16x8 b1 = *(const bf16x8*)&W1s[(t*16 + m16)*72 + 32 + quad*8];
-      accg[t] = __builtin_amdgcn_mfma_f32_16x16x32_bf16(a0, b0, accg[t], 0, 0, 0);
-      accg[t] = __builtin_amdgcn_mfma_f32_16x16x32_bf16(a1, b1, accg[t], 0, 0, 0);
-    }
-  }
-  {
-    bf16x8 a0 = *(const bf16x8*)&S2agg[(size_t)rowc*64 + quad*8];
-    bf16x8 a1 = *(const bf16x8*)&S2agg[(size_t)rowc*64 + 32 + quad*8];
-    #pragma unroll
-    for(int t = 0; t < 4; t++){
-      bf16x8 b0 = *(const bf16x8*)&W2s[(t*16 + m16)*72 + quad*8];
-      bf16x8 b1 = *(const bf16x8*)&W2s[(t*16 + m16)*72 + 32 + quad*8];
-      accs[t] = __builtin_amdgcn_mfma_f32_16x16x32_bf16(a0, b0, accs[t], 0, 0, 0);
-      accs[t] = __builtin_amdgcn_mfma_f32_16x16x32_bf16(a1, b1, accs[t], 0, 0, 0);
-    }
-  }
-  {
-    bf16x8 a0 = *(const bf16x8*)&s1[(size_t)rowc*64 + quad*8];
-    bf16x8 a1 = *(const bf16x8*)&s1[(size_t)rowc*64 + 32 + quad*8];
-    #pragma unroll
-    for(int t = 0; t < 4; t++){
-      bf16x8 b0 = *(const bf16x8*)&W3s[(t*16 + m16)*72 + quad*8];
-      bf16x8 b1 = *(const bf16x8*)&W3s[(t*16 + m16)*72 + 32 + quad*8];
-      accs[t] = __builtin_amdgcn_mfma_f32_16x16x32_bf16(a0, b0, accs[t], 0, 0, 0);
-      accs[t] = __builtin_amdgcn_mfma_f32_16x16x32_bf16(a1, b1, accs[t], 0, 0, 0);
-    }
-  }
-  float w0 = gatew[0], w1 = gatew[1], w2 = gatew[2];
-  int robase = blockIdx.x*64 + w*16 + quad*4;
-  float vs[4][4], n2[4] = {0,0,0,0};
-  #pragma unroll
-  for(int t = 0; t < 4; t++){
-    float bsv = bl2[t*16 + m16];
-    #pragma unroll
-    for(int r = 0; r < 4; r++){ vs[t][r] = accs[t][r] + bsv; n2[r] = fmaf(vs[t][r], vs[t][r], n2[r]); }
-  }
-  #pragma unroll
-  for(int d = 8; d >= 1; d >>= 1){
-    #pragma unroll
-    for(int r = 0; r < 4; r++) n2[r] += __shfl_xor(n2[r], d, 64);
-  }
-  float inv[4];
-  #pragma unroll
-  for(int r = 0; r < 4; r++) inv[r] = 1.0f / fmaxf(sqrtf(n2[r]), 1e-12f);
-  #pragma unroll
-  for(int t = 0; t < 4; t++){
-    int col = t*16 + m16;
-    float bg = gcn_b2[col], bt = gat_b2[col];
-    #pragma unroll
-    for(int r = 0; r < 4; r++){
-      int ro = robase + r;
-      if(ro < N){
-        float t2 = bflo((unsigned int)T2[(size_t)ro*64 + col]);
-        out[(size_t)ro*64 + col] = w0*(accg[t][r] + bg) + w1*(t2 + bt) + w2*vs[t][r]*inv[r];
+        float t2 = bflo((unsigned int)T2[((w<<4) + quad*4 + r)*72 + col]);
+        p.out[(size_t)ro*64 + col] = w0*(accg[t][r] + bg) + w1*(t2 + bt) + w2*vs[t][r]*inv[r];
       }
     }
   }
@@ -638,22 +577,10 @@
   float* adst1  = (float*)alloc((size_t)NN*4*4);
   float* asrc2  = (float*)alloc((size_t)NN*4);
   float* adst2  = (float*)alloc((size_t)NN*4);
-  float* wvE1   = (float*)alloc((size_t)NE*4*4);
-  float* rden1  = (float*)alloc((size_t)NN*4*4);
-  float* wvS1   = (float*)alloc((size_t)NN*4*4);
-  float* wvE2   = (float*)alloc((size_t)NE*4);
-  float* rden2  = (float*)alloc((size_t)NN*4);
-  float* wvS2   = (float*)alloc((size_t)NN*4);
-  unsigned short* xb     = (unsigned short*)alloc((size_t)NN*64*2);
-  unsigned short* z      = (unsigned short*)alloc((size_t)NN*256*2);
-  unsigned short* agcnx  = (unsigned short*)alloc((size_t)NN*64*2);
-  unsigned short* asagex = (unsigned short*)alloc((size_t)NN*64*2);
-  unsigned short* a1     = (unsigned short*)alloc((size_t)NN*64*2);
-  unsigned short* s1     = (unsigned short*)alloc((size_t)NN*64*2);
-  unsigned short* h2     = (unsigned short*)alloc((size_t)NN*64*2);
-  unsigned short* A2agg  = (unsigned short*)alloc((size_t)NN*64*2);
-  unsigned short* S2agg  = (unsigned short*)alloc((size_t)NN*64*2);
-  unsigned short* T2     = (unsigned short*)alloc((size_t)NN*64*2);
+  unsigned short* xb = (unsigned short*)alloc((size_t)NN*64*2);
+  unsigned short* a1 = (unsigned short*)alloc((size_t)NN*64*2);
+  unsigned short* s1 = (unsigned short*)alloc((size_t)NN*64*2);
+  unsigned short* h2 = (unsigned short*)alloc((size_t)NN*64*2);
   unsigned short* wb_gcn1 = (unsigned short*)alloc((size_t)64*64*2);
   unsigned short* wb_wl1  = (unsigned short*)alloc((size_t)64*64*2);
   unsigned short* wb_wr1  = (unsigned short*)alloc((size_t)64*64*2);
@@ -666,7 +593,6 @@
   hipMemsetAsync(cnt, 0, zbytes, stream);
 
   const int gN  = (NN + 63) / 64;
-  const int g4  = NN / 4;
   const int g16 = NN / 16;
   const int gA  = (NN + 255) / 256;
 
@@ -693,27 +619,28 @@
   k_gate  <<<1, 64, 0, stream>>>(gsum, gate_w1, gate_b1, gate_w2, gate_b2, gatew);
   k_fold1 <<<1, 256, 0, stream>>>(gat_w1, gat_as1, gat_ad1, wsd);
   k_attdotx<<<g16, 256, 0, stream>>>(xb, wsd, asrc1, adst1, NN);
-  k_edgew1<<<g4, 256, 0, stream>>>(asrc1, adst1, offs, cnt, csr, wvE1, rden1, wvS1, NN);
-
-  k_aggx<<<g4, 256, 0, stream>>>(xb, wvE1, rden1, wvS1, dis, invc, offs, cnt, csr,
-                                 z, agcnx, asagex, NN);
-
-  {
-    FSP p = {};
+
+  {
+    M1P p = {};
+    p.xb = xb; p.asrc1 = asrc1; p.adst1 = adst1;
+    p.offs = offs; p.cnt = cnt; p.csr = csr; p.dis = dis; p.invc = invc;
+    p.wb_gcn1 = wb_gcn1; p.gcn_b1 = gcn_b1; p.bn_gamma = bn_gamma; p.bn_beta = bn_beta;
+    p.wb_wl1 = wb_wl1; p.sage_bl1 = sage_bl1; p.wb_wr1 = wb_wr1;
+    p.wb_gat1 = wb_gat1; p.gat_b1 = gat_b1;
+    p.wb_gat2 = wb_gat2; p.gat_as2 = gat_as2; p.gat_ad2 = gat_ad2;
+    p.a1 = a1; p.s1 = s1; p.h2 = h2; p.asrc2 = asrc2; p.adst2 = adst2;
     p.N = NN;
-    p.z = z; p.wb1 = wb_gat1; p.b1 = gat_b1;
-    p.wb2 = wb_gat2; p.as2 = gat_as2; p.ad2 = gat_ad2;
-    p.h2 = h2; p.asrc2 = asrc2; p.adst2 = adst2;
-    p.mm[0] = {agcnx, wb_gcn1, nullptr, nullptr, a1, gcn_b1, bn_gamma, bn_beta, 1};
-    p.mm[1] = {asagex, wb_wl1, xb, wb_wr1, s1, sage_bl1, nullptr, nullptr, 3};
-    k_fused1<<<dim3(gN,3), 256, 0, stream>>>(p);
-  }
-
-  k_edgew2<<<g4, 256, 0, stream>>>(asrc2, adst2, offs, cnt, csr, wvE2, rden2, wvS2, NN);
-
-  k_aggf<<<g4, 256, 0, stream>>>(a1, s1, h2, wvE2, rden2, wvS2, dis, invc,
-                                 offs, cnt, csr, A2agg, S2agg, T2, NN);
-
-  k_mm_final<<<gN, 256, 0, stream>>>(A2agg, wb_gcn2, gcn_b2, S2agg, wb_wl2, sage_bl2,
-                                     s1, wb_wr2, T2, gat_b2, gatew, out, NN);
-}
+    k_mega1<<<gN, 256, 0, stream>>>(p);
+  }
+
+  {
+    M2P p = {};
+    p.a1 = a1; p.s1 = s1; p.h2 = h2; p.asrc2 = asrc2; p.adst2 = adst2;
+    p.offs = offs; p.cnt = cnt; p.csr = csr; p.dis = dis; p.invc = invc;
+    p.wb_gcn2 = wb_gcn2; p.gcn_b2 = gcn_b2;
+    p.wb_wl2 = wb_wl2; p.bl2 = sage_bl2; p.wb_wr2 = wb_wr2;
+    p.gat_b2 = gat_b2; p.gatew = gatew;
+    p.out = out; p.N = NN;
+    k_mega2<<<gN, 256, 0, stream>>>(p);
+  }
+}
```

Measured after the change: 427.1 us. 1.18x slower.
